# Kernel tuning notes

Hardware: AMD Instinct MI355X
Metric: run time of the kernel (lower is better)

## Reference

```python
import jax, jax.numpy as jnp
import numpy as np

D_MODEL = 256; N_LAYERS = 4; INPUT_LEN = 15
D_INNER = 512; D_STATE = 16; D_CONV = 4; DT_RANK = 16
BATCH = 4; SEQ = 2048; EPS = 1e-5

def _ln(x, w, b):
    m = jnp.mean(x, -1, keepdims=True)
    v = jnp.var(x, -1, keepdims=True)
    return (x - m) * jax.lax.rsqrt(v + EPS) * w + b

def _silu(x):
    return x * jax.nn.sigmoid(x)

def _mixer(h, inW, cw, cb, xpW, dtW, dtb, A_log, Dp, opW):
    # h: [B,L,d_model]
    xz = h @ inW.T                      # [B,L,2*D_INNER]
    xh, z = jnp.split(xz, 2, axis=-1)
    # causal depthwise conv1d
    xc = jnp.transpose(xh, (0, 2, 1))   # [B,D,L]
    xc = jax.lax.conv_general_dilated(xc, cw, (1,), [(D_CONV - 1, 0)],
                                      feature_group_count=D_INNER,
                                      dimension_numbers=('NCH', 'OIH', 'NCH'))
    xc = xc + cb[None, :, None]
    xh = _silu(jnp.transpose(xc, (0, 2, 1)))  # [B,L,D]
    dbl = xh @ xpW.T                    # [B,L,DT_RANK+2N]
    dt = dbl[..., :DT_RANK]
    Bm = dbl[..., DT_RANK:DT_RANK + D_STATE]
    C = dbl[..., DT_RANK + D_STATE:]
    dt = jax.nn.softplus(dt @ dtW.T + dtb)    # [B,L,D]
    A = -jnp.exp(A_log)                       # [D,N]
    dA = jnp.exp(dt[..., None] * A)           # [B,L,D,N]
    dBu = dt[..., None] * Bm[:, :, None, :] * xh[..., None]  # [B,L,D,N]
    def step(hst, inp):
        dA_t, dBu_t, C_t = inp
        hst = dA_t * hst + dBu_t
        y = jnp.einsum('bdn,bn->bd', hst, C_t)
        return hst, y
    h0 = jnp.zeros((xh.shape[0], D_INNER, D_STATE), xh.dtype)
    _, ys = jax.lax.scan(step, h0, (jnp.transpose(dA, (1, 0, 2, 3)),
                                    jnp.transpose(dBu, (1, 0, 2, 3)),
                                    jnp.transpose(C, (1, 0, 2))))
    y = jnp.transpose(ys, (1, 0, 2)) + Dp * xh
    y = y * _silu(z)
    return y @ opW.T

def setup_inputs():
    key = jax.random.key(0)
    ks = jax.random.split(key, 8)
    s = 0.02
    return {
        'x_src': jax.random.normal(ks[0], (BATCH, SEQ, INPUT_LEN), jnp.float32),
        'single_eval_pos': 1024,
        'in_W': jax.random.normal(ks[1], (D_MODEL, INPUT_LEN)) * s,
        'norm_w': jnp.ones((N_LAYERS, D_MODEL)),
        'norm_b': jnp.zeros((N_LAYERS, D_MODEL)),
        'inproj_W': jax.random.normal(ks[2], (N_LAYERS, 2 * D_INNER, D_MODEL)) * s,
        'conv_w': jax.random.normal(ks[3], (N_LAYERS, D_INNER, 1, D_CONV)) * 0.2,
        'conv_b': jnp.zeros((N_LAYERS, D_INNER)),
        'xproj_W': jax.random.normal(ks[4], (N_LAYERS, DT_RANK + 2 * D_STATE, D_INNER)) * s,
        'dtproj_W': jax.random.normal(ks[5], (N_LAYERS, D_INNER, DT_RANK)) * 0.1,
        'dtproj_b': jnp.log(jnp.expm1(jnp.full((N_LAYERS, D_INNER), 0.01))),
        'A_log': jnp.log(jnp.broadcast_to(jnp.arange(1, D_STATE + 1, dtype=jnp.float32), (N_LAYERS, D_INNER, D_STATE)) + 0.0),
        'D_param': jnp.ones((N_LAYERS, D_INNER)),
        'outproj_W': jax.random.normal(ks[6], (N_LAYERS, D_MODEL, D_INNER)) * s,
        'out_W': jax.random.normal(ks[7], (1, D_MODEL)) * s,
    }

def reference(x_src, single_eval_pos, in_W, norm_w, norm_b, inproj_W, conv_w, conv_b, xproj_W, dtproj_W, dtproj_b, A_log, D_param, outproj_W, out_W):
    h = x_src @ in_W.T                  # [B,L,d_model]
    res = None
    for i in range(N_LAYERS):
        res = h if res is None else h + res
        hn = _ln(res, norm_w[i], norm_b[i])
        h = _mixer(hn, inproj_W[i], conv_w[i], conv_b[i], xproj_W[i],
                   dtproj_W[i], dtproj_b[i], A_log[i], D_param[i], outproj_W[i])
    # backbone returns hidden_states directly (norm_f defined but not applied)
    return h @ out_W.T                  # [B,L,1]
```

## Files before the change

### kernel.cpp

```cpp
#include <hip/hip_runtime.h>

#define B_   4
#define T_   2048
#define BT_  8192
#define INL  15
#define DM   256
#define DI   512
#define DX   1024
#define DS_  16
#define DR_  16
#define NO_  48
#define NL   4
#define NC_  128
#define LCH  16

typedef short bf16x8 __attribute__((ext_vector_type(8)));
typedef float f32x4  __attribute__((ext_vector_type(4)));

__device__ __forceinline__ float sigmoidf_(float x){
    return __builtin_amdgcn_rcpf(1.f + __expf(-x));
}
__device__ __forceinline__ float softplusf_(float x){
    return fmaxf(x, 0.f) + __logf(1.f + __expf(-fabsf(x)));
}

__device__ __forceinline__ unsigned short f2bf(float x){
    union { float f; unsigned u; } v; v.f = x;
    unsigned r = (v.u + 0x7FFFu + ((v.u >> 16) & 1u)) >> 16;
    return (unsigned short)r;
}
__device__ __forceinline__ float bf2f(unsigned short h){
    union { unsigned u; float f; } v; v.u = ((unsigned)h) << 16;
    return v.f;
}

__device__ __forceinline__ void ld16(const float* __restrict__ p, float* v){
    const float4* q = (const float4*)p;
    float4 x0=q[0],x1=q[1],x2=q[2],x3=q[3];
    v[0]=x0.x; v[1]=x0.y; v[2]=x0.z; v[3]=x0.w;
    v[4]=x1.x; v[5]=x1.y; v[6]=x1.z; v[7]=x1.w;
    v[8]=x2.x; v[9]=x2.y; v[10]=x2.z; v[11]=x2.w;
    v[12]=x3.x; v[13]=x3.y; v[14]=x3.z; v[15]=x3.w;
}
__device__ __forceinline__ void st16(float* __restrict__ p, const float* v){
    float4* q = (float4*)p;
    q[0] = make_float4(v[0],v[1],v[2],v[3]);
    q[1] = make_float4(v[4],v[5],v[6],v[7]);
    q[2] = make_float4(v[8],v[9],v[10],v[11]);
    q[3] = make_float4(v[12],v[13],v[14],v[15]);
}

__global__ void k_cvtW3(const float* __restrict__ W0, unsigned short* __restrict__ h0,
                        unsigned short* __restrict__ l0, int n0,
                        const float* __restrict__ W1, unsigned short* __restrict__ h1,
                        unsigned short* __restrict__ l1, int n1,
                        const float* __restrict__ W2, unsigned short* __restrict__ h2,
                        unsigned short* __restrict__ l2, int n2){
    int g = blockIdx.x*256 + threadIdx.x;
    const float* W; unsigned short *hi, *lo; int idx;
    if(g < n0){ W = W0; hi = h0; lo = l0; idx = g; }
    else if(g < n0+n1){ W = W1; hi = h1; lo = l1; idx = g - n0; }
    else if(g < n0+n1+n2){ W = W2; hi = h2; lo = l2; idx = g - n0 - n1; }
    else return;
    float4 v = ((const float4*)W)[idx];
    ushort4 h, l;
    h.x = f2bf(v.x); l.x = f2bf(v.x - bf2f(h.x));
    h.y = f2bf(v.y); l.y = f2bf(v.y - bf2f(h.y));
    h.z = f2bf(v.z); l.z = f2bf(v.z - bf2f(h.z));
    h.w = f2bf(v.w); l.w = f2bf(v.w - bf2f(h.w));
    ((ushort4*)hi)[idx] = h;
    ((ushort4*)lo)[idx] = l;
}

__global__ void k_wcomb(const float* __restrict__ opW, const float* __restrict__ outW,
                        float* __restrict__ cw){
    int k = blockIdx.x*256 + threadIdx.x;
    float s = 0.f;
#pragma unroll 8
    for(int m=0;m<DM;m++) s += outW[m]*opW[(size_t)m*DI + k];
    cw[k] = s;
}

__global__ void k_inln(const float* __restrict__ x, const float* __restrict__ W,
                       float* __restrict__ res,
                       unsigned short* __restrict__ hnhi, unsigned short* __restrict__ hnlo,
                       const float* __restrict__ w, const float* __restrict__ b){
    int wv = threadIdx.x >> 6, lane = threadIdx.x & 63;
    int bt = blockIdx.x*4 + wv;
    const float* xr = x + bt*INL;
    float xl[INL];
#pragma unroll
    for(int k=0;k<INL;k++) xl[k] = xr[k];
    float4 v;
    float* vv = (float*)&v;
#pragma unroll
    for(int j=0;j<4;j++){
        int m = lane*4 + j;
        const float* wr = W + m*INL;
        float acc = 0.f;
#pragma unroll
        for(int k=0;k<INL;k++) acc += xl[k]*wr[k];
        vv[j] = acc;
    }
    ((float4*)(res + (size_t)bt*DM))[lane] = v;
    float s  = v.x+v.y+v.z+v.w;
    float ss = v.x*v.x+v.y*v.y+v.z*v.z+v.w*v.w;
#pragma unroll
    for(int m=1;m<64;m<<=1){ s += __shfl_xor(s,m); ss += __shfl_xor(ss,m); }
    float mean = s*(1.f/DM);
    float var  = ss*(1.f/DM) - mean*mean;
    float inv  = rsqrtf(var + 1e-5f);
    float4 wt = ((const float4*)w)[lane];
    float4 bs = ((const float4*)b)[lane];
    float4 o;
    o.x = (v.x-mean)*inv*wt.x + bs.x;
    o.y = (v.y-mean)*inv*wt.y + bs.y;
    o.z = (v.z-mean)*inv*wt.z + bs.z;
    o.w = (v.w-mean)*inv*wt.w + bs.w;
    ushort4 hh, ll;
    hh.x = f2bf(o.x); ll.x = f2bf(o.x - bf2f(hh.x));
    hh.y = f2bf(o.y); ll.y = f2bf(o.y - bf2f(hh.y));
    hh.z = f2bf(o.z); ll.z = f2bf(o.z - bf2f(hh.z));
    hh.w = f2bf(o.w); ll.w = f2bf(o.w - bf2f(hh.w));
    ((ushort4*)(hnhi + (size_t)bt*DM))[lane] = hh;
    ((ushort4*)(hnlo + (size_t)bt*DM))[lane] = ll;
}

__global__ void k_resln(const float* __restrict__ h, float* __restrict__ res,
                        unsigned short* __restrict__ hnhi, unsigned short* __restrict__ hnlo,
                        const float* __restrict__ w, const float* __restrict__ b, int addRes){
    int wv = threadIdx.x >> 6, lane = threadIdx.x & 63;
    int bt = blockIdx.x*4 + wv;
    float4 v = ((const float4*)(h + (size_t)bt*DM))[lane];
    if(addRes){
        float4 r = ((const float4*)(res + (size_t)bt*DM))[lane];
        v.x+=r.x; v.y+=r.y; v.z+=r.z; v.w+=r.w;
    }
    ((float4*)(res + (size_t)bt*DM))[lane] = v;
    float s  = v.x+v.y+v.z+v.w;
    float ss = v.x*v.x+v.y*v.y+v.z*v.z+v.w*v.w;
#pragma unroll
    for(int m=1;m<64;m<<=1){ s += __shfl_xor(s,m); ss += __shfl_xor(ss,m); }
    float mean = s*(1.f/DM);
    float var  = ss*(1.f/DM) - mean*mean;
    float inv  = rsqrtf(var + 1e-5f);
    float4 wt = ((const float4*)w)[lane];
    float4 bs = ((const float4*)b)[lane];
    float4 o;
    o.x = (v.x-mean)*inv*wt.x + bs.x;
    o.y = (v.y-mean)*inv*wt.y + bs.y;
    o.z = (v.z-mean)*inv*wt.z + bs.z;
    o.w = (v.w-mean)*inv*wt.w + bs.w;
    ushort4 hh, ll;
    hh.x = f2bf(o.x); ll.x = f2bf(o.x - bf2f(hh.x));
    hh.y = f2bf(o.y); ll.y = f2bf(o.y - bf2f(hh.y));
    hh.z = f2bf(o.z); ll.z = f2bf(o.z - bf2f(hh.z));
    hh.w = f2bf(o.w); ll.w = f2bf(o.w - bf2f(hh.w));
    ((ushort4*)(hnhi + (size_t)bt*DM))[lane] = hh;
    ((ushort4*)(hnlo + (size_t)bt*DM))[lane] = ll;
}

template<int BM,int BN>
__global__ void __launch_bounds__(256) k_gemm_bf3(
    const unsigned short* __restrict__ Ahi, const unsigned short* __restrict__ Alo,
    const unsigned short* __restrict__ Bhi, const unsigned short* __restrict__ Blo,
    float* __restrict__ C, int M, int N, int K)
{
    constexpr int LDP = 40;
    constexpr int WM = BM/2, WN = BN/2;
    constexpr int MI_ = WM/16, NI_ = WN/16;
    __shared__ unsigned short sAh[BM*LDP], sAl[BM*LDP], sBh[BN*LDP], sBl[BN*LDP];
    int tid  = threadIdx.x;
    int wave = tid >> 6, lane = tid & 63;
    int wm0  = (wave >> 1) * WM, wn0 = (wave & 1) * WN;
    int m0   = blockIdx.y * BM, n0 = blockIdx.x * BN;
    int lr   = lane & 15;
    int kq   = (lane >> 4) * 8;
    int quad4 = (lane >> 4) * 4;

    f32x4 acc[MI_][NI_];
#pragma unroll
    for(int i=0;i<MI_;i++)
#pragma unroll
        for(int j=0;j<NI_;j++) acc[i][j] = (f32x4){0.f,0.f,0.f,0.f};

    for(int k0=0;k0<K;k0+=32){
#pragma unroll
        for(int i=tid;i<BM*4;i+=256){
            int r = i>>2, cg = (i&3)*8;
            size_t go = (size_t)(m0+r)*K + k0 + cg;
            *(float4*)(&sAh[r*LDP + cg]) = *(const float4*)(Ahi + go);
            *(float4*)(&sAl[r*LDP + cg]) = *(const float4*)(Alo + go);
        }
#pragma unroll
        for(int i=tid;i<BN*4;i+=256){
            int r = i>>2, cg = (i&3)*8;
            size_t go = (size_t)(n0+r)*K + k0 + cg;
            *(float4*)(&sBh[r*LDP + cg]) = *(const float4*)(Bhi + go);
            *(float4*)(&sBl[r*LDP + cg]) = *(const float4*)(Blo + go);
        }
        __syncthreads();
        bf16x8 ah[MI_], al[MI_], bh[NI_], bl[NI_];
#pragma unroll
        for(int mi=0;mi<MI_;mi++){
            int ro = (wm0 + mi*16 + lr)*LDP + kq;
            ah[mi] = *(const bf16x8*)(&sAh[ro]);
            al[mi] = *(const bf16x8*)(&sAl[ro]);
        }
#pragma unroll
        for(int ni=0;ni<NI_;ni++){
            int ro = (wn0 + ni*16 + lr)*LDP + kq;
            bh[ni] = *(const bf16x8*)(&sBh[ro]);
            bl[ni] = *(const bf16x8*)(&sBl[ro]);
        }
#pragma unroll
        for(int mi=0;mi<MI_;mi++)
#pragma unroll
            for(int ni=0;ni<NI_;ni++){
                acc[mi][ni] = __builtin_amdgcn_mfma_f32_16x16x32_bf16(ah[mi], bh[ni], acc[mi][ni], 0,0,0);
                acc[mi][ni] = __builtin_amdgcn_mfma_f32_16x16x32_bf16(ah[mi], bl[ni], acc[mi][ni], 0,0,0);
                acc[mi][ni] = __builtin_amdgcn_mfma_f32_16x16x32_bf16(al[mi], bh[ni], acc[mi][ni], 0,0,0);
            }
        __syncthreads();
    }
#pragma unroll
    for(int mi=0;mi<MI_;mi++)
#pragma unroll
        for(int ni=0;ni<NI_;ni++){
            int col = n0 + wn0 + ni*16 + lr;
#pragma unroll
            for(int r=0;r<4;r++){
                int row = m0 + wm0 + mi*16 + quad4 + r;
                C[(size_t)row*N + col] = acc[mi][ni][r];
            }
        }
}

template<int BM,int BN>
__global__ void __launch_bounds__(256) k_gemm_pk(
    const unsigned* __restrict__ Apk,
    const unsigned short* __restrict__ Bhi, const unsigned short* __restrict__ Blo,
    float* __restrict__ C, int M, int N, int K)
{
    constexpr int LDP = 40;
    constexpr int WM = BM/2, WN = BN/2;
    constexpr int MI_ = WM/16, NI_ = WN/16;
    __shared__ unsigned short sAh[BM*LDP], sAl[BM*LDP], sBh[BN*LDP], sBl[BN*LDP];
    int tid  = threadIdx.x;
    int wave = tid >> 6, lane = tid & 63;
    int wm0  = (wave >> 1) * WM, wn0 = (wave & 1) * WN;
    int m0   = blockIdx.y * BM, n0 = blockIdx.x * BN;
    int lr   = lane & 15;
    int kq   = (lane >> 4) * 8;
    int quad4 = (lane >> 4) * 4;

    f32x4 acc[MI_][NI_];
#pragma unroll
    for(int i=0;i<MI_;i++)
#pragma unroll
        for(int j=0;j<NI_;j++) acc[i][j] = (f32x4){0.f,0.f,0.f,0.f};

    for(int k0=0;k0<K;k0+=32){
#pragma unroll
        for(int i=tid;i<BM*2;i+=256){
            int r = i>>1, hf = (i&1)*16;
            const uint4* yp = (const uint4*)(Apk + (size_t)(m0+r)*K + k0 + hf);
#pragma unroll
            for(int q=0;q<4;q++){
                uint4 p = yp[q];
                ushort4 H, L;
                H.x=(unsigned short)p.x;  L.x=(unsigned short)(p.x>>16);
                H.y=(unsigned short)p.y;  L.y=(unsigned short)(p.y>>16);
                H.z=(unsigned short)p.z;  L.z=(unsigned short)(p.z>>16);
                H.w=(unsigned short)p.w;  L.w=(unsigned short)(p.w>>16);
                *(ushort4*)(&sAh[r*LDP + hf + q*4]) = H;
                *(ushort4*)(&sAl[r*LDP + hf + q*4]) = L;
            }
        }
#pragma unroll
        for(int i=tid;i<BN*4;i+=256){
            int r = i>>2, cg = (i&3)*8;
            size_t go = (size_t)(n0+r)*K + k0 + cg;
            *(float4*)(&sBh[r*LDP + cg]) = *(const float4*)(Bhi + go);
            *(float4*)(&sBl[r*LDP + cg]) = *(const float4*)(Blo + go);
        }
        __syncthreads();
        bf16x8 ah[MI_], al[MI_], bh[NI_], bl[NI_];
#pragma unroll
        for(int mi=0;mi<MI_;mi++){
            int ro = (wm0 + mi*16 + lr)*LDP + kq;
            ah[mi] = *(const bf16x8*)(&sAh[ro]);
            al[mi] = *(const bf16x8*)(&sAl[ro]);
        }
#pragma unroll
        for(int ni=0;ni<NI_;ni++){
            int ro = (wn0 + ni*16 + lr)*LDP + kq;
            bh[ni] = *(const bf16x8*)(&sBh[ro]);
            bl[ni] = *(const bf16x8*)(&sBl[ro]);
        }
#pragma unroll
        for(int mi=0;mi<MI_;mi++)
#pragma unroll
            for(int ni=0;ni<NI_;ni++){
                acc[mi][ni] = __builtin_amdgcn_mfma_f32_16x16x32_bf16(ah[mi], bh[ni], acc[mi][ni], 0,0,0);
                acc[mi][ni] = __builtin_amdgcn_mfma_f32_16x16x32_bf16(ah[mi], bl[ni], acc[mi][ni], 0,0,0);
                acc[mi][ni] = __builtin_amdgcn_mfma_f32_16x16x32_bf16(al[mi], bh[ni], acc[mi][ni], 0,0,0);
            }
        __syncthreads();
    }
#pragma unroll
    for(int mi=0;mi<MI_;mi++)
#pragma unroll
        for(int ni=0;ni<NI_;ni++){
            int col = n0 + wn0 + ni*16 + lr;
#pragma unroll
            for(int r=0;r<4;r++){
                int row = m0 + wm0 + mi*16 + quad4 + r;
                C[(size_t)row*N + col] = acc[mi][ni][r];
            }
        }
}

__global__ void __launch_bounds__(512) k_convxp2(
    const float* __restrict__ xz, const float* __restrict__ cw, const float* __restrict__ cb,
    const unsigned short* __restrict__ Bhi, const unsigned short* __restrict__ Blo,
    const float* __restrict__ dtW, const float* __restrict__ dtbias,
    const float* __restrict__ A_log,
    float* __restrict__ xh, float* __restrict__ dbl,
    float* __restrict__ S, float* __restrict__ sdt)
{
    __shared__ unsigned short sAh[16*520], sAl[16*520];
    __shared__ float sP[6][16][20];
    __shared__ float sD[16*52];

    int tid = threadIdx.x;
    int wave = tid >> 6, lane = tid & 63;
    int lr = lane & 15, kq = (lane>>4)*8, quad4 = (lane>>4)*4;
    int m0 = blockIdx.x * LCH;
    int d  = tid;
    int nt = wave >> 1, kh = wave & 1;

    float xv[19];
    {
        int rbase = m0 - 3;
        bool mask0 = ((m0 & (T_-1)) == 0);
#pragma unroll
        for(int j=0;j<19;j++)
            xv[j] = (mask0 && j<3) ? 0.f : xz[(size_t)(rbase+j)*DX + d];
    }
    float a_[16]; ld16(A_log + (size_t)d*16, a_);
    float wr_[16]; ld16(dtW + (size_t)d*16, wr_);
    float bsv = dtbias[d];
    float4 w4 = *(const float4*)(cw + d*4);
    float bias = cb[d];
    float vh[16];
#pragma unroll
    for(int t=0;t<16;t++){
        float a = bias + w4.x*xv[t] + w4.y*xv[t+1] + w4.z*xv[t+2] + w4.w*xv[t+3];
        float v = a * sigmoidf_(a);
        vh[t] = v;
        xh[(size_t)(m0+t)*DI + d] = v;
        unsigned short hh = f2bf(v);
        sAh[t*520 + d] = hh;
        sAl[t*520 + d] = f2bf(v - bf2f(hh));
    }
    __syncthreads();

    if(wave < 6){
        const unsigned short* bhp = Bhi + (size_t)(nt*16 + lr)*DI + kh*256 + kq;
        const unsigned short* blp = Blo + (size_t)(nt*16 + lr)*DI + kh*256 + kq;
        f32x4 acc = {0.f,0.f,0.f,0.f};
#pragma unroll 4
        for(int ks=0;ks<8;ks++){
            int ao = lr*520 + kh*256 + ks*32 + kq;
            bf16x8 ah = *(const bf16x8*)(&sAh[ao]);
            bf16x8 al = *(const bf16x8*)(&sAl[ao]);
            bf16x8 bh = *(const bf16x8*)(bhp + ks*32);
            bf16x8 bl = *(const bf16x8*)(blp + ks*32);
            acc = __builtin_amdgcn_mfma_f32_16x16x32_bf16(ah, bh, acc, 0,0,0);
            acc = __builtin_amdgcn_mfma_f32_16x16x32_bf16(ah, bl, acc, 0,0,0);
            acc = __builtin_amdgcn_mfma_f32_16x16x32_bf16(al, bh, acc, 0,0,0);
        }
#pragma unroll
        for(int r=0;r<4;r++) sP[wave][quad4+r][lr] = acc[r];
    }
    __syncthreads();

    for(int i=tid;i<768;i+=512){
        int t = i/48, n = i - t*48;
        int nt2 = n >> 4, nn = n & 15;
        float v = sP[nt2*2][t][nn] + sP[nt2*2+1][t][nn];
        dbl[(size_t)(m0+t)*48 + n] = v;
        sD[t*52 + n] = v;
    }
    __syncthreads();

#pragma unroll
    for(int n=0;n<16;n++) a_[n] = -__expf(a_[n]);
    int b = m0 >> 11;
    int c = (m0 & (T_-1)) >> 4;
    float st_[16];
#pragma unroll
    for(int n=0;n<16;n++) st_[n] = 0.f;
    float sd = 0.f;
#pragma unroll 4
    for(int t=0;t<16;t++){
        float dl[16]; ld16(&sD[t*52], dl);
        float bv[16]; ld16(&sD[t*52 + 16], bv);
        float pre = bsv;
#pragma unroll
        for(int r=0;r<16;r++) pre += dl[r]*wr_[r];
        float dtv = softplusf_(pre);
        float dx = dtv*vh[t];
        sd += dtv;
#pragma unroll
        for(int n=0;n<16;n++) st_[n] = __expf(dtv*a_[n])*st_[n] + dx*bv[n];
    }
    st16(S + (((size_t)b*NC_ + c)*DI + d)*16, st_);
    sdt[((size_t)b*NC_ + c)*DI + d] = sd;
}

__global__ void k_scan2(const float* __restrict__ S, const float* __restrict__ sdt,
                        const float* __restrict__ A_log, float* __restrict__ Hinit){
    int g = blockIdx.x*256 + threadIdx.x;
    int b = g >> 13;
    int dn = g & 8191;
    int d = dn >> 4;
    float a = -__expf(A_log[dn]);
    float H = 0.f;
    for(int c0=0;c0<NC_;c0+=8){
        float sv[8], gv[8];
#pragma unroll
        for(int j=0;j<8;j++){
            sv[j] = S[((size_t)(b*NC_ + c0 + j))*8192 + dn];
            gv[j] = sdt[(size_t)(b*NC_ + c0 + j)*DI + d];
        }
#pragma unroll
        for(int j=0;j<8;j++){
            size_t o = ((size_t)(b*NC_ + c0 + j))*8192 + dn;
            Hinit[o] = H;
            H = __expf(gv[j]*a)*H + sv[j];
        }
    }
}

__global__ void __launch_bounds__(256) k_scan3(
    const float* __restrict__ dbl, const float* __restrict__ xh, const float* __restrict__ xz,
    const float* __restrict__ A_log, const float* __restrict__ Dpar,
    const float* __restrict__ dtW, const float* __restrict__ dtbias,
    const float* __restrict__ Hinit, unsigned* __restrict__ Y)
{
    __shared__ float sbc[16*52];
    int tid = threadIdx.x;
    int c = blockIdx.y, b = blockIdx.z;
    int m0 = b*T_ + c*LCH;
    if(tid < 192){
        int t = tid/12, s = tid - t*12;
        *(float4*)(&sbc[t*52 + s*4]) = *(const float4*)(dbl + (size_t)(m0+t)*48 + s*4);
    }
    __syncthreads();
    int d = blockIdx.x*256 + tid;
    float xhp[16], zvp[16];
#pragma unroll
    for(int t=0;t<16;t++){
        xhp[t] = xh[(size_t)(m0+t)*DI + d];
        zvp[t] = xz[(size_t)(m0+t)*DX + DI + d];
    }
    float a_[16]; ld16(A_log + (size_t)d*16, a_);
#pragma unroll
    for(int n=0;n<16;n++) a_[n] = -__expf(a_[n]);
    float wr_[16]; ld16(dtW + (size_t)d*16, wr_);
    float bsv = dtbias[d];
    float st_[16]; ld16(Hinit + (((size_t)b*NC_ + c)*DI + d)*16, st_);
    float Dp = Dpar[d];
#pragma unroll 2
    for(int t=0;t<LCH;t++){
        int bt = m0 + t;
        float dl[16]; ld16(&sbc[t*52], dl);
        float bv[16]; ld16(&sbc[t*52 + 16], bv);
        float cv[16]; ld16(&sbc[t*52 + 32], cv);
        float pre = bsv;
#pragma unroll
        for(int r=0;r<16;r++) pre += dl[r]*wr_[r];
        float dtv = softplusf_(pre);
        float xhv = xhp[t];
        float dx = dtv*xhv;
        float y = 0.f;
#pragma unroll
        for(int n=0;n<16;n++){
            st_[n] = __expf(dtv*a_[n])*st_[n] + dx*bv[n];
            y += st_[n]*cv[n];
        }
        float zv = zvp[t];
        y += Dp*xhv;
        y = y * zv * sigmoidf_(zv);
        unsigned short hh = f2bf(y);
        unsigned short ll = f2bf(y - bf2f(hh));
        Y[(size_t)bt*DI + d] = (unsigned)hh | ((unsigned)ll << 16);
    }
}

__global__ void k_gemv(const unsigned* __restrict__ Y, const float* __restrict__ cw,
                       float* __restrict__ out){
    int wv = threadIdx.x >> 6, lane = threadIdx.x & 63;
    int bt = blockIdx.x*4 + wv;
    const uint4* yp = (const uint4*)(Y + (size_t)bt*DI);
    uint4 p0 = yp[lane*2], p1 = yp[lane*2+1];
    float4 c0 = ((const float4*)cw)[lane*2], c1 = ((const float4*)cw)[lane*2+1];
    float s = 0.f;
    s += (bf2f((unsigned short)p0.x) + bf2f((unsigned short)(p0.x>>16))) * c0.x;
    s += (bf2f((unsigned short)p0.y) + bf2f((unsigned short)(p0.y>>16))) * c0.y;
    s += (bf2f((unsigned short)p0.z) + bf2f((unsigned short)(p0.z>>16))) * c0.z;
    s += (bf2f((unsigned short)p0.w) + bf2f((unsigned short)(p0.w>>16))) * c0.w;
    s += (bf2f((unsigned short)p1.x) + bf2f((unsigned short)(p1.x>>16))) * c1.x;
    s += (bf2f((unsigned short)p1.y) + bf2f((unsigned short)(p1.y>>16))) * c1.y;
    s += (bf2f((unsigned short)p1.z) + bf2f((unsigned short)(p1.z>>16))) * c1.z;
    s += (bf2f((unsigned short)p1.w) + bf2f((unsigned short)(p1.w>>16))) * c1.w;
#pragma unroll
    for(int m=1;m<64;m<<=1) s += __shfl_xor(s,m);
    if(lane==0) out[bt] = s;
}

extern "C" void kernel_launch(void* const* d_in, const int* in_sizes, int n_in,
                              void* d_out, int out_size, void* d_ws, size_t ws_size,
                              hipStream_t stream){
    const float* x_src    = (const float*)d_in[0];
    const float* in_W     = (const float*)d_in[2];
    const float* norm_w   = (const float*)d_in[3];
    const float* norm_b   = (const float*)d_in[4];
    const float* inproj_W = (const float*)d_in[5];
    const float* conv_w   = (const float*)d_in[6];
    const float* conv_b   = (const float*)d_in[7];
    const float* xproj_W  = (const float*)d_in[8];
    const float* dtproj_W = (const float*)d_in[9];
    const float* dtproj_b = (const float*)d_in[10];
    const float* A_log    = (const float*)d_in[11];
    const float* D_param  = (const float*)d_in[12];
    const float* outproj_W= (const float*)d_in[13];
    const float* out_W    = (const float*)d_in[14];

    float* ws  = (float*)d_ws;
    float* h    = ws;
    float* res  = h    + (size_t)BT_*DM;
    float* xz   = res  + (size_t)BT_*DM;
    float* xh   = xz   + (size_t)BT_*DX;
    float* dbl  = xh   + (size_t)BT_*DI;
    float* sdtb = dbl  + (size_t)BT_*48;
    float* Sbuf = sdtb + (size_t)B_*NC_*DI;
    float* Hbuf = Sbuf + (size_t)B_*NC_*DI*DS_;
    unsigned short* us = (unsigned short*)(Hbuf + (size_t)B_*NC_*DI*DS_);
    unsigned short* WhiIn  = us;
    unsigned short* WloIn  = WhiIn  + (size_t)NL*DX*DM;
    unsigned short* WhiOut = WloIn  + (size_t)NL*DX*DM;
    unsigned short* WloOut = WhiOut + (size_t)NL*DM*DI;
    unsigned short* WhiXp  = WloOut + (size_t)NL*DM*DI;
    unsigned short* WloXp  = WhiXp  + (size_t)NL*NO_*DI;
    unsigned short* hnhi   = WloXp  + (size_t)NL*NO_*DI;
    unsigned short* hnlo   = hnhi   + (size_t)BT_*DM;
    unsigned*       ybuf   = (unsigned*)(hnlo + (size_t)BT_*DM);
    float*          cwb    = (float*)(ybuf + (size_t)BT_*DI);

    int n0 = NL*DX*DM/4, n1 = NL*DM*DI/4, n2 = NL*NO_*DI/4;
    k_cvtW3<<<(n0+n1+n2 + 255)/256, 256, 0, stream>>>(
        inproj_W,  WhiIn,  WloIn,  n0,
        outproj_W, WhiOut, WloOut, n1,
        xproj_W,   WhiXp,  WloXp,  n2);
    k_wcomb<<<2, 256, 0, stream>>>(outproj_W + (size_t)3*DM*DI, out_W, cwb);
    k_inln<<<BT_/4, 256, 0, stream>>>(x_src, in_W, res, hnhi, hnlo, norm_w, norm_b);
    for(int i=0;i<NL;i++){
        if(i > 0)
            k_resln<<<BT_/4, 256, 0, stream>>>(h, res, hnhi, hnlo, norm_w + i*DM, norm_b + i*DM, 1);
        k_gemm_bf3<128,128><<<dim3(DX/128, BT_/128), 256, 0, stream>>>(
            hnhi, hnlo, WhiIn + (size_t)i*DX*DM, WloIn + (size_t)i*DX*DM, xz, BT_, DX, DM);
        k_convxp2<<<BT_/LCH, 512, 0, stream>>>(xz, conv_w + i*DI*4, conv_b + i*DI,
            WhiXp + (size_t)i*NO_*DI, WloXp + (size_t)i*NO_*DI,
            dtproj_W + (size_t)i*DI*DR_, dtproj_b + i*DI,
            A_log + (size_t)i*DI*DS_, xh, dbl, Sbuf, sdtb);
        k_scan2<<<B_*DI*DS_/256, 256, 0, stream>>>(Sbuf, sdtb, A_log + (size_t)i*DI*DS_, Hbuf);
        k_scan3<<<dim3(2, NC_, B_), 256, 0, stream>>>(dbl, xh, xz,
            A_log + (size_t)i*DI*DS_, D_param + i*DI,
            dtproj_W + (size_t)i*DI*DR_, dtproj_b + i*DI, Hbuf, ybuf);
        if(i < NL-1)
            k_gemm_pk<128,64><<<dim3(DM/64, BT_/128), 256, 0, stream>>>(
                ybuf, WhiOut + (size_t)i*DM*DI, WloOut + (size_t)i*DM*DI, h, BT_, DM, DI);
    }
    k_gemv<<<BT_/4, 256, 0, stream>>>(ybuf, cwb, (float*)d_out);
}
```

Measured before the change: 561.7 us.

## Recompute conv output in scan, fuse final gemv into last-layer scan

Stops writing the conv+SiLU activation xh to global memory. The scan kernel now recomputes it from xz using the conv weights, trading a 16x512 fp32 store and reload per chunk for a few redundant FMAs and sigmoids. On the last layer a new 512-thread scan kernel dots y with the combined output weights and reduces across waves, which removes the ybuf write and the separate gemv launch. The last residual store is also skipped because nothing reads it.

```diff
diff --git a/kernel.cpp b/kernel.cpp
--- a/kernel.cpp
+++ b/kernel.cpp
@@ -128,15 +128,16 @@
 
 __global__ void k_resln(const float* __restrict__ h, float* __restrict__ res,
                         unsigned short* __restrict__ hnhi, unsigned short* __restrict__ hnlo,
-                        const float* __restrict__ w, const float* __restrict__ b, int addRes){
+                        const float* __restrict__ w, const float* __restrict__ b, int storeRes){
     int wv = threadIdx.x >> 6, lane = threadIdx.x & 63;
     int bt = blockIdx.x*4 + wv;
     float4 v = ((const float4*)(h + (size_t)bt*DM))[lane];
-    if(addRes){
+    {
         float4 r = ((const float4*)(res + (size_t)bt*DM))[lane];
         v.x+=r.x; v.y+=r.y; v.z+=r.z; v.w+=r.w;
     }
-    ((float4*)(res + (size_t)bt*DM))[lane] = v;
+    if(storeRes)
+        ((float4*)(res + (size_t)bt*DM))[lane] = v;
     float s  = v.x+v.y+v.z+v.w;
     float ss = v.x*v.x+v.y*v.y+v.z*v.z+v.w*v.w;
 #pragma unroll
@@ -326,7 +327,7 @@
     const unsigned short* __restrict__ Bhi, const unsigned short* __restrict__ Blo,
     const float* __restrict__ dtW, const float* __restrict__ dtbias,
     const float* __restrict__ A_log,
-    float* __restrict__ xh, float* __restrict__ dbl,
+    float* __restrict__ dbl,
     float* __restrict__ S, float* __restrict__ sdt)
 {
     __shared__ unsigned short sAh[16*520], sAl[16*520];
@@ -359,7 +360,6 @@
         float a = bias + w4.x*xv[t] + w4.y*xv[t+1] + w4.z*xv[t+2] + w4.w*xv[t+3];
         float v = a * sigmoidf_(a);
         vh[t] = v;
-        xh[(size_t)(m0+t)*DI + d] = v;
         unsigned short hh = f2bf(v);
         sAh[t*520 + d] = hh;
         sAl[t*520 + d] = f2bf(v - bf2f(hh));
@@ -445,7 +445,8 @@
 }
 
 __global__ void __launch_bounds__(256) k_scan3(
-    const float* __restrict__ dbl, const float* __restrict__ xh, const float* __restrict__ xz,
+    const float* __restrict__ dbl, const float* __restrict__ xz,
+    const float* __restrict__ cvw, const float* __restrict__ cvb,
     const float* __restrict__ A_log, const float* __restrict__ Dpar,
     const float* __restrict__ dtW, const float* __restrict__ dtbias,
     const float* __restrict__ Hinit, unsigned* __restrict__ Y)
@@ -460,11 +461,24 @@
     }
     __syncthreads();
     int d = blockIdx.x*256 + tid;
-    float xhp[16], zvp[16];
+    float xv[19];
+    {
+        int rbase = m0 - 3;
+        bool mask0 = (c == 0);
+#pragma unroll
+        for(int j=0;j<19;j++)
+            xv[j] = (mask0 && j<3) ? 0.f : xz[(size_t)(rbase+j)*DX + d];
+    }
+    float zvp[16];
+#pragma unroll
+    for(int t=0;t<16;t++) zvp[t] = xz[(size_t)(m0+t)*DX + DI + d];
+    float4 w4 = *(const float4*)(cvw + d*4);
+    float bias = cvb[d];
+    float xhp[16];
 #pragma unroll
     for(int t=0;t<16;t++){
-        xhp[t] = xh[(size_t)(m0+t)*DI + d];
-        zvp[t] = xz[(size_t)(m0+t)*DX + DI + d];
+        float a = bias + w4.x*xv[t] + w4.y*xv[t+1] + w4.z*xv[t+2] + w4.w*xv[t+3];
+        xhp[t] = a * sigmoidf_(a);
     }
     float a_[16]; ld16(A_log + (size_t)d*16, a_);
 #pragma unroll
@@ -500,25 +514,85 @@
     }
 }
 
-__global__ void k_gemv(const unsigned* __restrict__ Y, const float* __restrict__ cw,
-                       float* __restrict__ out){
-    int wv = threadIdx.x >> 6, lane = threadIdx.x & 63;
-    int bt = blockIdx.x*4 + wv;
-    const uint4* yp = (const uint4*)(Y + (size_t)bt*DI);
-    uint4 p0 = yp[lane*2], p1 = yp[lane*2+1];
-    float4 c0 = ((const float4*)cw)[lane*2], c1 = ((const float4*)cw)[lane*2+1];
-    float s = 0.f;
-    s += (bf2f((unsigned short)p0.x) + bf2f((unsigned short)(p0.x>>16))) * c0.x;
-    s += (bf2f((unsigned short)p0.y) + bf2f((unsigned short)(p0.y>>16))) * c0.y;
-    s += (bf2f((unsigned short)p0.z) + bf2f((unsigned short)(p0.z>>16))) * c0.z;
-    s += (bf2f((unsigned short)p0.w) + bf2f((unsigned short)(p0.w>>16))) * c0.w;
-    s += (bf2f((unsigned short)p1.x) + bf2f((unsigned short)(p1.x>>16))) * c1.x;
-    s += (bf2f((unsigned short)p1.y) + bf2f((unsigned short)(p1.y>>16))) * c1.y;
-    s += (bf2f((unsigned short)p1.z) + bf2f((unsigned short)(p1.z>>16))) * c1.z;
-    s += (bf2f((unsigned short)p1.w) + bf2f((unsigned short)(p1.w>>16))) * c1.w;
-#pragma unroll
-    for(int m=1;m<64;m<<=1) s += __shfl_xor(s,m);
-    if(lane==0) out[bt] = s;
+__global__ void __launch_bounds__(512) k_scan3o(
+    const float* __restrict__ dbl, const float* __restrict__ xz,
+    const float* __restrict__ cvw, const float* __restrict__ cvb,
+    const float* __restrict__ A_log, const float* __restrict__ Dpar,
+    const float* __restrict__ dtW, const float* __restrict__ dtbias,
+    const float* __restrict__ Hinit, const float* __restrict__ cwc,
+    float* __restrict__ out)
+{
+    __shared__ float sbc[16*52];
+    __shared__ float sW[8][16];
+    int tid = threadIdx.x;
+    int c = blockIdx.x, b = blockIdx.y;
+    int m0 = b*T_ + c*LCH;
+    if(tid < 192){
+        int t = tid/12, s = tid - t*12;
+        *(float4*)(&sbc[t*52 + s*4]) = *(const float4*)(dbl + (size_t)(m0+t)*48 + s*4);
+    }
+    __syncthreads();
+    int d = tid;
+    int wave = tid >> 6, lane = tid & 63;
+    float xv[19];
+    {
+        int rbase = m0 - 3;
+        bool mask0 = (c == 0);
+#pragma unroll
+        for(int j=0;j<19;j++)
+            xv[j] = (mask0 && j<3) ? 0.f : xz[(size_t)(rbase+j)*DX + d];
+    }
+    float zvp[16];
+#pragma unroll
+    for(int t=0;t<16;t++) zvp[t] = xz[(size_t)(m0+t)*DX + DI + d];
+    float4 w4 = *(const float4*)(cvw + d*4);
+    float bias = cvb[d];
+    float xhp[16];
+#pragma unroll
+    for(int t=0;t<16;t++){
+        float a = bias + w4.x*xv[t] + w4.y*xv[t+1] + w4.z*xv[t+2] + w4.w*xv[t+3];
+        xhp[t] = a * sigmoidf_(a);
+    }
+    float a_[16]; ld16(A_log + (size_t)d*16, a_);
+#pragma unroll
+    for(int n=0;n<16;n++) a_[n] = -__expf(a_[n]);
+    float wr_[16]; ld16(dtW + (size_t)d*16, wr_);
+    float bsv = dtbias[d];
+    float st_[16]; ld16(Hinit + (((size_t)b*NC_ + c)*DI + d)*16, st_);
+    float Dp = Dpar[d];
+    float cwv = cwc[d];
+#pragma unroll 2
+    for(int t=0;t<LCH;t++){
+        float dl[16]; ld16(&sbc[t*52], dl);
+        float bv[16]; ld16(&sbc[t*52 + 16], bv);
+        float cv[16]; ld16(&sbc[t*52 + 32], cv);
+        float pre = bsv;
+#pragma unroll
+        for(int r=0;r<16;r++) pre += dl[r]*wr_[r];
+        float dtv = softplusf_(pre);
+        float xhv = xhp[t];
+        float dx = dtv*xhv;
+        float y = 0.f;
+#pragma unroll
+        for(int n=0;n<16;n++){
+            st_[n] = __expf(dtv*a_[n])*st_[n] + dx*bv[n];
+            y += st_[n]*cv[n];
+        }
+        float zv = zvp[t];
+        y += Dp*xhv;
+        y = y * zv * sigmoidf_(zv);
+        float s = y * cwv;
+#pragma unroll
+        for(int m=1;m<64;m<<=1) s += __shfl_xor(s,m);
+        if(lane==0) sW[wave][t] = s;
+    }
+    __syncthreads();
+    if(tid < 16){
+        float s = 0.f;
+#pragma unroll
+        for(int w=0;w<8;w++) s += sW[w][tid];
+        out[m0 + tid] = s;
+    }
 }
 
 extern "C" void kernel_launch(void* const* d_in, const int* in_sizes, int n_in,
@@ -543,8 +617,7 @@
     float* h    = ws;
     float* res  = h    + (size_t)BT_*DM;
     float* xz   = res  + (size_t)BT_*DM;
-    float* xh   = xz   + (size_t)BT_*DX;
-    float* dbl  = xh   + (size_t)BT_*DI;
+    float* dbl  = xz   + (size_t)BT_*DX;
     float* sdtb = dbl  + (size_t)BT_*48;
     float* Sbuf = sdtb + (size_t)B_*NC_*DI;
     float* Hbuf = Sbuf + (size_t)B_*NC_*DI*DS_;
@@ -569,20 +642,28 @@
     k_inln<<<BT_/4, 256, 0, stream>>>(x_src, in_W, res, hnhi, hnlo, norm_w, norm_b);
     for(int i=0;i<NL;i++){
         if(i > 0)
-            k_resln<<<BT_/4, 256, 0, stream>>>(h, res, hnhi, hnlo, norm_w + i*DM, norm_b + i*DM, 1);
+            k_resln<<<BT_/4, 256, 0, stream>>>(h, res, hnhi, hnlo,
+                norm_w + i*DM, norm_b + i*DM, (i < NL-1) ? 1 : 0);
         k_gemm_bf3<128,128><<<dim3(DX/128, BT_/128), 256, 0, stream>>>(
             hnhi, hnlo, WhiIn + (size_t)i*DX*DM, WloIn + (size_t)i*DX*DM, xz, BT_, DX, DM);
         k_convxp2<<<BT_/LCH, 512, 0, stream>>>(xz, conv_w + i*DI*4, conv_b + i*DI,
             WhiXp + (size_t)i*NO_*DI, WloXp + (size_t)i*NO_*DI,
             dtproj_W + (size_t)i*DI*DR_, dtproj_b + i*DI,
-            A_log + (size_t)i*DI*DS_, xh, dbl, Sbuf, sdtb);
+            A_log + (size_t)i*DI*DS_, dbl, Sbuf, sdtb);
         k_scan2<<<B_*DI*DS_/256, 256, 0, stream>>>(Sbuf, sdtb, A_log + (size_t)i*DI*DS_, Hbuf);
-        k_scan3<<<dim3(2, NC_, B_), 256, 0, stream>>>(dbl, xh, xz,
-            A_log + (size_t)i*DI*DS_, D_param + i*DI,
-            dtproj_W + (size_t)i*DI*DR_, dtproj_b + i*DI, Hbuf, ybuf);
-        if(i < NL-1)
+        if(i < NL-1){
+            k_scan3<<<dim3(2, NC_, B_), 256, 0, stream>>>(dbl, xz,
+                conv_w + i*DI*4, conv_b + i*DI,
+                A_log + (size_t)i*DI*DS_, D_param + i*DI,
+                dtproj_W + (size_t)i*DI*DR_, dtproj_b + i*DI, Hbuf, ybuf);
             k_gemm_pk<128,64><<<dim3(DM/64, BT_/128), 256, 0, stream>>>(
                 ybuf, WhiOut + (size_t)i*DM*DI, WloOut + (size_t)i*DM*DI, h, BT_, DM, DI);
-    }
-    k_gemv<<<BT_/4, 256, 0, stream>>>(ybuf, cwb, (float*)d_out);
-}
+        } else {
+            k_scan3o<<<dim3(NC_, B_), 512, 0, stream>>>(dbl, xz,
+                conv_w + i*DI*4, conv_b + i*DI,
+                A_log + (size_t)i*DI*DS_, D_param + i*DI,
+                dtproj_W + (size_t)i*DI*DR_, dtproj_b + i*DI, Hbuf, cwb,
+                (float*)d_out);
+        }
+    }
+}
```

Result: no change. 553.6 us (-1.4%).
